# Performance work log

Measured on AMD Instinct MI355X. Metric: run time of the kernel, lower is better.

The kernel has to match this reference:

```python
import jax, jax.numpy as jnp
import numpy as np

B, P, E, H = 2, 4096, 512, 8
D = E // H
EPS = 1e-5


def _layernorm2d(x, g, b):
    # LayerNorm over last two dims (patches, embed) jointly, per torch nn.LayerNorm([P, E])
    mu = jnp.mean(x, axis=(-2, -1), keepdims=True)
    var = jnp.mean(jnp.square(x - mu), axis=(-2, -1), keepdims=True)
    return (x - mu) * jax.lax.rsqrt(var + EPS) * g + b


def setup_inputs() -> dict:
    key = jax.random.key(0)
    ks = jax.random.split(key, 4)
    s_in = 1.0 / np.sqrt(E)
    s_hid = 1.0 / np.sqrt(3 * E)
    return {
        "x": jax.random.normal(ks[0], (B, P, E), dtype=jnp.float32),
        "g1": jnp.ones((P, E), jnp.float32),
        "b1": jnp.zeros((P, E), jnp.float32),
        "W1": jax.random.normal(ks[1], (3 * E, E), jnp.float32) * s_in,
        "g2": jnp.ones((P, E), jnp.float32),
        "b2": jnp.zeros((P, E), jnp.float32),
        "Wa": jax.random.normal(ks[2], (3 * E, E), jnp.float32) * s_in,
        "ba": jnp.zeros((3 * E,), jnp.float32),
        "Wb": jax.random.normal(ks[3], (E, 3 * E), jnp.float32) * s_hid,
        "bb": jnp.zeros((E,), jnp.float32),
    }


def reference(x, g1, b1, W1, g2, b2, Wa, ba, Wb, bb):
    # --- attention branch ---
    h = _layernorm2d(x, g1, b1)                      # [B,P,E]
    qkv = h @ W1.T                                   # [B,P,3E]
    qkv = qkv.reshape(B, P, 3, H, D).transpose(2, 0, 3, 1, 4)  # [3,B,H,P,D]
    q, k, v = qkv[0], qkv[1], qkv[2]
    scale = 1.0 / jnp.sqrt(jnp.float32(D))
    dp = jnp.einsum("bhqd,bhkd->bhqk", q, k) * scale  # [B,H,P,P]
    # NOTE: softmax over axis -2 (the query axis), as in the original code
    dp = jax.nn.softmax(dp, axis=-2)
    wv = jnp.einsum("bhqk,bhkd->bhqd", dp, v)        # [B,H,P,D]
    wv = wv.transpose(0, 2, 1, 3).reshape(B, P, E)   # [B,P,E]
    out1 = x + wv
    # --- MLP branch ---
    h2 = _layernorm2d(out1, g2, b2)
    h2 = jax.nn.gelu(h2 @ Wa.T + ba, approximate=False)
    h2 = jax.nn.gelu(h2 @ Wb.T + bb, approximate=False)
    return h2 + out1
```

## Files before the change

kernel.cpp:

```cpp
#include <hip/hip_runtime.h>
#include <math.h>

typedef __bf16 bf16x8 __attribute__((ext_vector_type(8)));
typedef float f32x4 __attribute__((ext_vector_type(4)));
typedef unsigned short u16;
typedef unsigned int u32;

__device__ __forceinline__ void gl_lds16(const void* g, void* l) {
  __builtin_amdgcn_global_load_lds(
      (const __attribute__((address_space(1))) void*)g,
      (__attribute__((address_space(3))) void*)l, 16, 0, 0);
}

__device__ __forceinline__ u16 f2bf(float x) {
  union { float f; u32 u; } v; v.f = x;
  u32 r = v.u + 0x7FFFu + ((v.u >> 16) & 1u);
  return (u16)(r >> 16);
}

__device__ __forceinline__ u32 pack_bf2(float a, float b) {
  union { float f; u32 u; } ua, ub; ua.f = a; ub.f = b;
  return ((ua.u + 0x8000u) >> 16) | ((ub.u + 0x8000u) & 0xFFFF0000u);
}

__device__ __forceinline__ float gelu_f(float v) {
  return 0.5f * v * (1.0f + erff(v * 0.7071067811865475f));
}

__global__ void castbf3(const float* __restrict__ s0, const float* __restrict__ s1,
                        const float* __restrict__ s2, u16* __restrict__ d0,
                        u16* __restrict__ d1, u16* __restrict__ d2) {
  int blk = blockIdx.x;
  const float* s; u16* d;
  if (blk < 768)       { s = s0; d = d0; }
  else if (blk < 1536) { s = s1; d = d1; blk -= 768; }
  else                 { s = s2; d = d2; blk -= 1536; }
  int i = blk * 256 + threadIdx.x;
  float4 v = ((const float4*)s)[i];
  uint2 o;
  o.x = (u32)f2bf(v.x) | ((u32)f2bf(v.y) << 16);
  o.y = (u32)f2bf(v.z) | ((u32)f2bf(v.w) << 16);
  ((uint2*)d)[i] = o;
}

__global__ void ln_reduce(const float* __restrict__ src, float2* __restrict__ part) {
  int b = blockIdx.y;
  const float4* p = (const float4*)(src + (size_t)b * 2097152 + (size_t)blockIdx.x * 16384);
  float s = 0.f, q = 0.f;
  #pragma unroll
  for (int i = 0; i < 16; i++) {
    float4 v = p[i * 256 + threadIdx.x];
    s += v.x + v.y + v.z + v.w;
    q += v.x * v.x + v.y * v.y + v.z * v.z + v.w * v.w;
  }
  #pragma unroll
  for (int off = 32; off; off >>= 1) { s += __shfl_down(s, off, 64); q += __shfl_down(q, off, 64); }
  __shared__ float ls[4], lq[4];
  int w = threadIdx.x >> 6;
  if ((threadIdx.x & 63) == 0) { ls[w] = s; lq[w] = q; }
  __syncthreads();
  if (threadIdx.x == 0)
    part[b * 128 + blockIdx.x] =
        make_float2(ls[0] + ls[1] + ls[2] + ls[3], lq[0] + lq[1] + lq[2] + lq[3]);
}

__global__ void ln_final(const float2* __restrict__ part, float2* __restrict__ stats) {
  int b = blockIdx.x, t = threadIdx.x;
  float2 a = part[b * 128 + t], c = part[b * 128 + 64 + t];
  float s = a.x + c.x, q = a.y + c.y;
  #pragma unroll
  for (int off = 32; off; off >>= 1) { s += __shfl_down(s, off, 64); q += __shfl_down(q, off, 64); }
  if (t == 0) {
    const float inv = 1.0f / 2097152.0f;
    float mu = s * inv, var = q * inv - mu * mu;
    stats[b] = make_float2(mu, rsqrtf(var + 1e-5f));
  }
}

__global__ void ln_apply(const float* __restrict__ src, const float* __restrict__ g,
                         const float* __restrict__ bta, const float2* __restrict__ stats,
                         u16* __restrict__ dst) {
  int i = blockIdx.x * 256 + threadIdx.x;
  int b = i >= 524288;
  float2 st = stats[b];
  int r = i - b * 524288;
  float4 v = ((const float4*)src)[i];
  float4 gv = ((const float4*)g)[r];
  float4 bv = ((const float4*)bta)[r];
  float h0 = (v.x - st.x) * st.y * gv.x + bv.x;
  float h1 = (v.y - st.x) * st.y * gv.y + bv.y;
  float h2 = (v.z - st.x) * st.y * gv.z + bv.z;
  float h3 = (v.w - st.x) * st.y * gv.w + bv.w;
  uint2 o;
  o.x = (u32)f2bf(h0) | ((u32)f2bf(h1) << 16);
  o.y = (u32)f2bf(h2) | ((u32)f2bf(h3) << 16);
  ((uint2*)dst)[i] = o;
}

template <int MODE>
__global__ __launch_bounds__(256, 2)
void gemm_bt(const u16* __restrict__ A, const u16* __restrict__ Bm,
             const float* __restrict__ bias, const float* __restrict__ res,
             float* __restrict__ outf, u16* __restrict__ outb,
             int M, int N, int K) {
  __shared__ u16 As[128 * 32], Bs[128 * 32];
  const int tid = threadIdx.x;
  const int m0 = blockIdx.y * 128, n0 = blockIdx.x * 128;
  const int lane = tid & 63, w = tid >> 6;
  const int wm = (w >> 1) * 64, wn = (w & 1) * 64;
  const int c = lane & 15, quad = lane >> 4;
  const int arow = tid >> 2, acol = (tid & 3) * 8;

  const u16* gA = A + (size_t)(m0 + arow) * K + acol;
  const u16* gB = Bm + (size_t)(n0 + arow) * K + acol;
  u16* lA = As + tid * 8;
  u16* lB = Bs + tid * 8;

  f32x4 acc[4][4] = {};
  for (int kt = 0; kt < K; kt += 32) {
    gl_lds16(gA, lA);
    gl_lds16(gA + (size_t)64 * K, lA + 64 * 32);
    gl_lds16(gB, lB);
    gl_lds16(gB + (size_t)64 * K, lB + 64 * 32);
    gA += 32; gB += 32;
    __syncthreads();
    bf16x8 af[4], bf[4];
    #pragma unroll
    for (int i = 0; i < 4; i++) {
      af[i] = *(const bf16x8*)&As[(wm + i * 16 + c) * 32 + quad * 8];
      bf[i] = *(const bf16x8*)&Bs[(wn + i * 16 + c) * 32 + quad * 8];
    }
    #pragma unroll
    for (int i = 0; i < 4; i++)
      #pragma unroll
      for (int j = 0; j < 4; j++)
        acc[i][j] = __builtin_amdgcn_mfma_f32_16x16x32_bf16(af[i], bf[j], acc[i][j], 0, 0, 0);
    __syncthreads();
  }
  #pragma unroll
  for (int i = 0; i < 4; i++) {
    const int row0 = m0 + wm + i * 16 + quad * 4;
    #pragma unroll
    for (int j = 0; j < 4; j++) {
      const int col = n0 + wn + j * 16 + c;
      #pragma unroll
      for (int r = 0; r < 4; r++) {
        float v = acc[i][j][r];
        size_t oi = (size_t)(row0 + r) * N + col;
        if (MODE == 0 && col < 512) v *= 0.125f;
        if (MODE == 1 || MODE == 2) v = gelu_f(v + bias[col]);
        if (MODE == 2) outf[oi] = v + res[oi];
        else           outb[oi] = f2bf(v);
      }
    }
  }
}

__global__ __launch_bounds__(256, 2)
void attn_pass1(const u16* __restrict__ qkv, float* __restrict__ rl) {
  const int tid = threadIdx.x;
  const int bh = blockIdx.y, b = bh >> 3, h = bh & 7;
  const int k0 = blockIdx.x * 128;
  const int lane = tid & 63, w = tid >> 6;
  const int wn = w * 32;
  const int c = lane & 15, quad = lane >> 4;

  bf16x8 bk[2][2];
  {
    const u16* Kg = qkv + ((size_t)(b * 4096 + k0 + wn + c)) * 1536 + 512 + h * 64 + quad * 8;
    #pragma unroll
    for (int j = 0; j < 2; j++)
      #pragma unroll
      for (int ks = 0; ks < 2; ks++)
        bk[j][ks] = *(const bf16x8*)(Kg + (size_t)j * 16 * 1536 + ks * 32);
  }
  const u16* Qg = qkv + ((size_t)(b * 4096 + c)) * 1536 + h * 64 + quad * 8;

  float s0 = 0.f, s1 = 0.f;
  for (int qt = 0; qt < 64; qt++) {
    f32x4 acc[4][2] = {};
    #pragma unroll
    for (int i4 = 0; i4 < 4; i4++) {
      const u16* qp = Qg + (size_t)(qt * 64 + i4 * 16) * 1536;
      bf16x8 a0 = *(const bf16x8*)(qp);
      bf16x8 a1 = *(const bf16x8*)(qp + 32);
      acc[i4][0] = __builtin_amdgcn_mfma_f32_16x16x32_bf16(a0, bk[0][0], acc[i4][0], 0, 0, 0);
      acc[i4][0] = __builtin_amdgcn_mfma_f32_16x16x32_bf16(a1, bk[0][1], acc[i4][0], 0, 0, 0);
      acc[i4][1] = __builtin_amdgcn_mfma_f32_16x16x32_bf16(a0, bk[1][0], acc[i4][1], 0, 0, 0);
      acc[i4][1] = __builtin_amdgcn_mfma_f32_16x16x32_bf16(a1, bk[1][1], acc[i4][1], 0, 0, 0);
    }
    #pragma unroll
    for (int i4 = 0; i4 < 4; i4++) {
      #pragma unroll
      for (int r = 0; r < 4; r++) {
        s0 += __expf(acc[i4][0][r]);
        s1 += __expf(acc[i4][1][r]);
      }
    }
  }
  s0 += __shfl_xor(s0, 16, 64); s0 += __shfl_xor(s0, 32, 64);
  s1 += __shfl_xor(s1, 16, 64); s1 += __shfl_xor(s1, 32, 64);
  if (quad == 0) {
    rl[(size_t)bh * 4096 + k0 + wn + c]      = 1.0f / s0;
    rl[(size_t)bh * 4096 + k0 + wn + 16 + c] = 1.0f / s1;
  }
}

__global__ void vtrans(const u16* __restrict__ qkv, const float* __restrict__ rl,
                       u16* __restrict__ vt) {
  __shared__ u16 t[64 * 66];
  int bh = blockIdx.y, p0 = blockIdx.x * 64;
  int b = bh >> 3, h = bh & 7;
  const u16* src = qkv + ((size_t)(b * 4096 + p0)) * 1536 + 1024 + h * 64;
  const float* rp = rl + (size_t)bh * 4096 + p0;
  int tid = threadIdx.x;
  #pragma unroll
  for (int j = 0; j < 16; j++) {
    int idx = j * 256 + tid;
    int p = idx >> 6, d = idx & 63;
    union { float f; u32 u; } uv;
    uv.u = ((u32)src[(size_t)p * 1536 + d]) << 16;
    t[d * 66 + p] = f2bf(uv.f * rp[p]);
  }
  __syncthreads();
  u16* dst = vt + (size_t)bh * 64 * 4096 + p0;
  #pragma unroll
  for (int j = 0; j < 16; j++) {
    int idx = j * 256 + tid;
    int d = idx >> 6, p = idx & 63;
    dst[(size_t)d * 4096 + p] = t[d * 66 + p];
  }
}

__global__ __launch_bounds__(256, 2)
void attn_pass2(const u16* __restrict__ qkv, const u16* __restrict__ vt,
                const float* __restrict__ x, float* __restrict__ out1) {
  __shared__ u16 Ks[2 * 128 * 32];
  __shared__ u16 Vs[4 * 64 * 32];
  __shared__ u16 Ps[4 * 128 * 32];
  const int tid = threadIdx.x;
  const int bh = blockIdx.y, b = bh >> 3, h = bh & 7;
  const int q0 = blockIdx.x * 128;
  const int lane = tid & 63, w = tid >> 6;
  const int wq = w * 32;
  const int c = lane & 15, quad = lane >> 4;
  const int arow = tid >> 2, acol = (tid & 3) * 8;

  bf16x8 bq[2][2];
  {
    const u16* Qg = qkv + ((size_t)(b * 4096 + q0 + wq + c)) * 1536 + h * 64 + quad * 8;
    #pragma unroll
    for (int j = 0; j < 2; j++)
      #pragma unroll
      for (int ks = 0; ks < 2; ks++)
        bq[j][ks] = *(const bf16x8*)(Qg + (size_t)j * 16 * 1536 + ks * 32);
  }
  const u16* Kg = qkv + ((size_t)(b * 4096)) * 1536 + 512 + h * 64;
  const u16* Vg = vt + (size_t)bh * 64 * 4096;

  f32x4 oacc[2][4] = {};
  for (int kt = 0; kt < 32; kt++) {
    const int k0 = kt * 128;
    #pragma unroll
    for (int ks = 0; ks < 2; ks++)
      #pragma unroll
      for (int rr = 0; rr < 128; rr += 64)
        gl_lds16(Kg + (size_t)(k0 + rr + arow) * 1536 + ks * 32 + acol,
                 Ks + ks * 4096 + (rr + arow) * 32 + acol);
    #pragma unroll
    for (int kp = 0; kp < 4; kp++)
      gl_lds16(Vg + (size_t)arow * 4096 + k0 + kp * 32 + acol,
               Vs + kp * 2048 + arow * 32 + acol);
    __syncthreads();

    #pragma unroll
    for (int ih = 0; ih < 2; ih++) {
      f32x4 sacc[4][2] = {};
      #pragma unroll
      for (int i4 = 0; i4 < 4; i4++) {
        const int i = ih * 4 + i4;
        bf16x8 af0 = *(const bf16x8*)&Ks[(i * 16 + c) * 32 + quad * 8];
        bf16x8 af1 = *(const bf16x8*)&Ks[4096 + (i * 16 + c) * 32 + quad * 8];
        sacc[i4][0] = __builtin_amdgcn_mfma_f32_16x16x32_bf16(af0, bq[0][0], sacc[i4][0], 0, 0, 0);
        sacc[i4][0] = __builtin_amdgcn_mfma_f32_16x16x32_bf16(af1, bq[0][1], sacc[i4][0], 0, 0, 0);
        sacc[i4][1] = __builtin_amdgcn_mfma_f32_16x16x32_bf16(af0, bq[1][0], sacc[i4][1], 0, 0, 0);
        sacc[i4][1] = __builtin_amdgcn_mfma_f32_16x16x32_bf16(af1, bq[1][1], sacc[i4][1], 0, 0, 0);
      }
      #pragma unroll
      for (int i4 = 0; i4 < 4; i4++) {
        const int i = ih * 4 + i4;
        #pragma unroll
        for (int j = 0; j < 2; j++) {
          const int qloc = wq + j * 16 + c;
          const int sl = ((i & 1) * 4 + quad) ^ (((qloc >> 1) & 3) << 1);
          u16* pp = Ps + (i >> 1) * 4096 + qloc * 32 + sl * 4;
          float e0 = __expf(sacc[i4][j][0]);
          float e1 = __expf(sacc[i4][j][1]);
          float e2 = __expf(sacc[i4][j][2]);
          float e3 = __expf(sacc[i4][j][3]);
          uint2 pk;
          pk.x = pack_bf2(e0, e1);
          pk.y = pack_bf2(e2, e3);
          *(uint2*)pp = pk;
        }
      }
    }
    #pragma unroll
    for (int ksb = 0; ksb < 4; ksb++) {
      bf16x8 pf[2], vf[4];
      #pragma unroll
      for (int i2 = 0; i2 < 2; i2++) {
        const int qloc = wq + i2 * 16 + c;
        const int blk = quad ^ ((qloc >> 1) & 3);
        pf[i2] = *(const bf16x8*)&Ps[ksb * 4096 + qloc * 32 + blk * 8];
      }
      #pragma unroll
      for (int j2 = 0; j2 < 4; j2++)
        vf[j2] = *(const bf16x8*)&Vs[ksb * 2048 + (j2 * 16 + c) * 32 + quad * 8];
      #pragma unroll
      for (int i2 = 0; i2 < 2; i2++)
        #pragma unroll
        for (int j2 = 0; j2 < 4; j2++)
          oacc[i2][j2] = __builtin_amdgcn_mfma_f32_16x16x32_bf16(pf[i2], vf[j2], oacc[i2][j2], 0, 0, 0);
    }
    __syncthreads();
  }
  #pragma unroll
  for (int i2 = 0; i2 < 2; i2++)
    #pragma unroll
    for (int j2 = 0; j2 < 4; j2++)
      #pragma unroll
      for (int r = 0; r < 4; r++) {
        const int q = q0 + wq + i2 * 16 + quad * 4 + r;
        const int d = j2 * 16 + c;
        size_t oi = ((size_t)(b * 4096 + q)) * 512 + h * 64 + d;
        out1[oi] = x[oi] + oacc[i2][j2][r];
      }
}

extern "C" void kernel_launch(void* const* d_in, const int* in_sizes, int n_in,
                              void* d_out, int out_size, void* d_ws, size_t ws_size,
                              hipStream_t stream) {
  const float* x  = (const float*)d_in[0];
  const float* g1 = (const float*)d_in[1];
  const float* b1 = (const float*)d_in[2];
  const float* W1 = (const float*)d_in[3];
  const float* g2 = (const float*)d_in[4];
  const float* b2 = (const float*)d_in[5];
  const float* Wa = (const float*)d_in[6];
  const float* ba = (const float*)d_in[7];
  const float* Wb = (const float*)d_in[8];
  const float* bb = (const float*)d_in[9];
  float* out = (float*)d_out;

  char* ws = (char*)d_ws;
  u16* w1b   = (u16*)(ws);
  u16* wab   = (u16*)(ws + 1572864);
  u16* wbb   = (u16*)(ws + 3145728);
  u16* h1    = (u16*)(ws + 4718592);
  u16* qkv   = (u16*)(ws + 13107200);
  u16* vt    = (u16*)(ws + 38273024);
  u16* h2    = (u16*)(ws + 46661632);
  u16* mid   = (u16*)(ws + 55050240);
  float* rl  = (float*)(ws + 80216064);
  float* o1  = (float*)(ws + 80478208);
  float2* part  = (float2*)(ws + 97255424);
  float2* stats = (float2*)(ws + 97257472);

  castbf3<<<2304, 256, 0, stream>>>(W1, Wa, Wb, w1b, wab, wbb);

  ln_reduce<<<dim3(128, 2), 256, 0, stream>>>(x, part);
  ln_final<<<2, 64, 0, stream>>>(part, stats);
  ln_apply<<<4096, 256, 0, stream>>>(x, g1, b1, stats, h1);

  gemm_bt<0><<<dim3(12, 64), 256, 0, stream>>>(h1, w1b, nullptr, nullptr, nullptr, qkv,
                                               8192, 1536, 512);
  attn_pass1<<<dim3(32, 16), 256, 0, stream>>>(qkv, rl);
  vtrans<<<dim3(64, 16), 256, 0, stream>>>(qkv, rl, vt);
  attn_pass2<<<dim3(32, 16), 256, 0, stream>>>(qkv, vt, x, o1);

  ln_reduce<<<dim3(128, 2), 256, 0, stream>>>(o1, part);
  ln_final<<<2, 64, 0, stream>>>(part, stats);
  ln_apply<<<4096, 256, 0, stream>>>(o1, g2, b2, stats, h2);

  gemm_bt<1><<<dim3(12, 64), 256, 0, stream>>>(h2, wab, ba, nullptr, nullptr, mid,
                                               8192, 1536, 512);
  gemm_bt<2><<<dim3(4, 64), 256, 0, stream>>>(mid, wbb, bb, o1, out, nullptr,
                                              8192, 512, 1536);
}
```

Before: 454.1 us.

## Stage Q tiles through LDS, split attn_pass1 over query halves, use exp2

attn_pass1 now stages Q tiles into double-buffered shared memory with direct global-to-LDS loads instead of scattered per-lane global reads. The query range is split across two blocks (grid z=2) to raise parallelism, and a small combine kernel sums the partial column sums and takes the reciprocal. The q scale is folded to include log2(e) so both attention passes can use the hardware exp2 instruction. The cost is an extra kernel launch and a scratch buffer that reuses the mid region, plus higher occupancy pressure from the new launch bounds.

```diff
diff --git a/kernel.cpp b/kernel.cpp
--- a/kernel.cpp
+++ b/kernel.cpp
@@ -21,6 +21,14 @@
 __device__ __forceinline__ u32 pack_bf2(float a, float b) {
   union { float f; u32 u; } ua, ub; ua.f = a; ub.f = b;
   return ((ua.u + 0x8000u) >> 16) | ((ub.u + 0x8000u) & 0xFFFF0000u);
+}
+
+__device__ __forceinline__ float expfast(float x) {
+#if __has_builtin(__builtin_amdgcn_exp2f)
+  return __builtin_amdgcn_exp2f(x);
+#else
+  return exp2f(x);
+#endif
 }
 
 __device__ __forceinline__ float gelu_f(float v) {
@@ -147,7 +155,7 @@
       for (int r = 0; r < 4; r++) {
         float v = acc[i][j][r];
         size_t oi = (size_t)(row0 + r) * N + col;
-        if (MODE == 0 && col < 512) v *= 0.125f;
+        if (MODE == 0 && col < 512) v *= 0.1803368801111204f;
         if (MODE == 1 || MODE == 2) v = gelu_f(v + bias[col]);
         if (MODE == 2) outf[oi] = v + res[oi];
         else           outb[oi] = f2bf(v);
@@ -156,14 +164,16 @@
   }
 }
 
-__global__ __launch_bounds__(256, 2)
-void attn_pass1(const u16* __restrict__ qkv, float* __restrict__ rl) {
+__global__ __launch_bounds__(256, 4)
+void attn_pass1(const u16* __restrict__ qkv, float* __restrict__ rlpart) {
+  __shared__ u16 Qs[2][2 * 128 * 32];
   const int tid = threadIdx.x;
   const int bh = blockIdx.y, b = bh >> 3, h = bh & 7;
   const int k0 = blockIdx.x * 128;
   const int lane = tid & 63, w = tid >> 6;
   const int wn = w * 32;
   const int c = lane & 15, quad = lane >> 4;
+  const int arow = tid >> 2, acol = (tid & 3) * 8;
 
   bf16x8 bk[2][2];
   {
@@ -174,36 +184,55 @@
       for (int ks = 0; ks < 2; ks++)
         bk[j][ks] = *(const bf16x8*)(Kg + (size_t)j * 16 * 1536 + ks * 32);
   }
-  const u16* Qg = qkv + ((size_t)(b * 4096 + c)) * 1536 + h * 64 + quad * 8;
-
+  const u16* Qg = qkv + ((size_t)(b * 4096 + blockIdx.z * 2048)) * 1536 + h * 64;
+
+  #define STAGE_Q(t)                                                              \
+    {                                                                             \
+      u16* dst = Qs[(t) & 1];                                                     \
+      const u16* src = Qg + (size_t)((t) * 128) * 1536;                           \
+      _Pragma("unroll")                                                           \
+      for (int ks = 0; ks < 2; ks++)                                              \
+        _Pragma("unroll")                                                         \
+        for (int rr = 0; rr < 128; rr += 64)                                      \
+          gl_lds16(src + (size_t)(rr + arow) * 1536 + ks * 32 + acol,             \
+                   dst + ks * 4096 + (rr + arow) * 32 + acol);                    \
+    }
+
+  STAGE_Q(0);
   float s0 = 0.f, s1 = 0.f;
-  for (int qt = 0; qt < 64; qt++) {
-    f32x4 acc[4][2] = {};
-    #pragma unroll
-    for (int i4 = 0; i4 < 4; i4++) {
-      const u16* qp = Qg + (size_t)(qt * 64 + i4 * 16) * 1536;
-      bf16x8 a0 = *(const bf16x8*)(qp);
-      bf16x8 a1 = *(const bf16x8*)(qp + 32);
-      acc[i4][0] = __builtin_amdgcn_mfma_f32_16x16x32_bf16(a0, bk[0][0], acc[i4][0], 0, 0, 0);
-      acc[i4][0] = __builtin_amdgcn_mfma_f32_16x16x32_bf16(a1, bk[0][1], acc[i4][0], 0, 0, 0);
-      acc[i4][1] = __builtin_amdgcn_mfma_f32_16x16x32_bf16(a0, bk[1][0], acc[i4][1], 0, 0, 0);
-      acc[i4][1] = __builtin_amdgcn_mfma_f32_16x16x32_bf16(a1, bk[1][1], acc[i4][1], 0, 0, 0);
-    }
-    #pragma unroll
-    for (int i4 = 0; i4 < 4; i4++) {
+  for (int t = 0; t < 16; t++) {
+    __syncthreads();
+    if (t + 1 < 16) STAGE_Q(t + 1);
+    const u16* buf = Qs[t & 1];
+    #pragma unroll
+    for (int i = 0; i < 8; i++) {
+      bf16x8 a0 = *(const bf16x8*)&buf[(i * 16 + c) * 32 + quad * 8];
+      bf16x8 a1 = *(const bf16x8*)&buf[4096 + (i * 16 + c) * 32 + quad * 8];
+      f32x4 acc0 = {}, acc1 = {};
+      acc0 = __builtin_amdgcn_mfma_f32_16x16x32_bf16(a0, bk[0][0], acc0, 0, 0, 0);
+      acc0 = __builtin_amdgcn_mfma_f32_16x16x32_bf16(a1, bk[0][1], acc0, 0, 0, 0);
+      acc1 = __builtin_amdgcn_mfma_f32_16x16x32_bf16(a0, bk[1][0], acc1, 0, 0, 0);
+      acc1 = __builtin_amdgcn_mfma_f32_16x16x32_bf16(a1, bk[1][1], acc1, 0, 0, 0);
       #pragma unroll
       for (int r = 0; r < 4; r++) {
-        s0 += __expf(acc[i4][0][r]);
-        s1 += __expf(acc[i4][1][r]);
-      }
-    }
-  }
+        s0 += expfast(acc0[r]);
+        s1 += expfast(acc1[r]);
+      }
+    }
+  }
+  #undef STAGE_Q
   s0 += __shfl_xor(s0, 16, 64); s0 += __shfl_xor(s0, 32, 64);
   s1 += __shfl_xor(s1, 16, 64); s1 += __shfl_xor(s1, 32, 64);
   if (quad == 0) {
-    rl[(size_t)bh * 4096 + k0 + wn + c]      = 1.0f / s0;
-    rl[(size_t)bh * 4096 + k0 + wn + 16 + c] = 1.0f / s1;
-  }
+    float* rp = rlpart + ((size_t)blockIdx.z * 16 + bh) * 4096 + k0 + wn;
+    rp[c] = s0;
+    rp[16 + c] = s1;
+  }
+}
+
+__global__ void rl_comb(const float* __restrict__ part, float* __restrict__ rl) {
+  int i = blockIdx.x * 256 + threadIdx.x;
+  rl[i] = 1.0f / (part[i] + part[65536 + i]);
 }
 
 __global__ void vtrans(const u16* __restrict__ qkv, const float* __restrict__ rl,
@@ -294,10 +323,10 @@
           const int qloc = wq + j * 16 + c;
           const int sl = ((i & 1) * 4 + quad) ^ (((qloc >> 1) & 3) << 1);
           u16* pp = Ps + (i >> 1) * 4096 + qloc * 32 + sl * 4;
-          float e0 = __expf(sacc[i4][j][0]);
-          float e1 = __expf(sacc[i4][j][1]);
-          float e2 = __expf(sacc[i4][j][2]);
-          float e3 = __expf(sacc[i4][j][3]);
+          float e0 = expfast(sacc[i4][j][0]);
+          float e1 = expfast(sacc[i4][j][1]);
+          float e2 = expfast(sacc[i4][j][2]);
+          float e3 = expfast(sacc[i4][j][3]);
           uint2 pk;
           pk.x = pack_bf2(e0, e1);
           pk.y = pack_bf2(e2, e3);
@@ -366,6 +395,7 @@
   float* o1  = (float*)(ws + 80478208);
   float2* part  = (float2*)(ws + 97255424);
   float2* stats = (float2*)(ws + 97257472);
+  float* rlpart = (float*)(ws + 55050240);
 
   castbf3<<<2304, 256, 0, stream>>>(W1, Wa, Wb, w1b, wab, wbb);
 
@@ -375,7 +405,8 @@
 
   gemm_bt<0><<<dim3(12, 64), 256, 0, stream>>>(h1, w1b, nullptr, nullptr, nullptr, qkv,
                                                8192, 1536, 512);
-  attn_pass1<<<dim3(32, 16), 256, 0, stream>>>(qkv, rl);
+  attn_pass1<<<dim3(32, 16, 2), 256, 0, stream>>>(qkv, rlpart);
+  rl_comb<<<256, 256, 0, stream>>>(rlpart, rl);
   vtrans<<<dim3(64, 16), 256, 0, stream>>>(qkv, rl, vt);
   attn_pass2<<<dim3(32, 16), 256, 0, stream>>>(qkv, vt, x, o1);
 
```

New measurement: 384.0 us. 15.4% less time.
